# Kernel tuning notes

Hardware: AMD Instinct MI355X
Metric: run time of the kernel (lower is better)

The kernel has to match this reference:

```python
import jax, jax.numpy as jnp
import numpy as np

B, S, D, U = 8, 2048, 512, 512
L0, L1 = 128, 128  # limit_context (left, right)


def setup_inputs() -> dict:
    key = jax.random.key(0)
    ks = jax.random.split(key, 7)
    scale = 1.0 / np.sqrt(D).astype(np.float32)
    return {
        "x": jax.random.normal(ks[0], (B, S, D), dtype=jnp.float32),
        "Wq": jax.random.normal(ks[1], (D, U), dtype=jnp.float32) * scale,
        "Wk": jax.random.normal(ks[2], (D, U), dtype=jnp.float32) * scale,
        "Wv": jax.random.normal(ks[3], (D, U), dtype=jnp.float32) * scale,
        "bq": jnp.zeros((U,), dtype=jnp.float32),
        "bk": jnp.zeros((U,), dtype=jnp.float32),
        "bv": jnp.zeros((U,), dtype=jnp.float32),
    }


def reference(x, Wq, Wk, Wv, bq, bk, bv):
    # Linear projections for query / key / value (shared input x)
    q = x @ Wq + bq  # [B,S,U]
    k = x @ Wk + bk  # [B,S,U]
    v = x @ Wv + bv  # [B,S,U]

    inv_sqrt_dv = jnp.float32(1.0 / np.sqrt(U))
    scores = jnp.einsum("bqd,bkd->bqk", q, k) * inv_sqrt_dv  # [B,S,S]

    # Sliding-window mask: key j visible to query i iff i-L0 <= j <= i+L1.
    # Equivalent to the original per-step softmax over values[:, start:end].
    i = jnp.arange(S)[:, None]
    j = jnp.arange(S)[None, :]
    window = (j >= i - L0) & (j <= i + L1)  # [S,S]
    neg_inf = jnp.finfo(scores.dtype).min
    scores = jnp.where(window[None], scores, neg_inf)

    attn = jax.nn.softmax(scores, axis=-1)  # [B,S,S]
    return jnp.einsum("bqk,bkd->bqd", attn, v)  # [B,S,U]
```

## Files before the change

### kernel.cpp

```cpp
#include <hip/hip_runtime.h>

#define BATCH 8
#define S_LEN 2048
#define DDIM 512
#define UDIM 512
#define WIN_L 128
#define WIN_R 128
#define KP 520
#define VP 40
#define PP 296

typedef _Float16 f16;
typedef __attribute__((ext_vector_type(8))) _Float16 f16x8;
typedef __attribute__((ext_vector_type(4))) _Float16 f16x4;
typedef __attribute__((ext_vector_type(4))) float f32x4;

__device__ __forceinline__ void gload_lds16(const void* g, void* l) {
  __builtin_amdgcn_global_load_lds((const __attribute__((address_space(1))) void*)g,
                                   (__attribute__((address_space(3))) void*)l, 16, 0, 0);
}

__global__ void cast_f32_f16(const float* __restrict__ in, f16* __restrict__ out, int n) {
  int i = (blockIdx.x * blockDim.x + threadIdx.x) * 4;
  if (i < n) {
    float4 v = *(const float4*)(in + i);
    f16x4 o;
    o[0] = (f16)v.x; o[1] = (f16)v.y; o[2] = (f16)v.z; o[3] = (f16)v.w;
    *(f16x4*)(out + i) = o;
  }
}

__global__ void transpose_w(const float* __restrict__ Wq, const float* __restrict__ Wk,
                            const float* __restrict__ Wv, f16* __restrict__ WT) {
  const float* W = blockIdx.z == 0 ? Wq : (blockIdx.z == 1 ? Wk : Wv);
  f16* WTz = WT + (size_t)blockIdx.z * DDIM * UDIM;
  __shared__ float t[32][33];
  int tx = threadIdx.x & 31, ty = threadIdx.x >> 5;
  int n0 = blockIdx.x * 32, k0 = blockIdx.y * 32;
  for (int i = 0; i < 4; i++) {
    int r = ty * 4 + i;
    t[r][tx] = W[(size_t)(k0 + r) * UDIM + n0 + tx];
  }
  __syncthreads();
  for (int i = 0; i < 4; i++) {
    int r = ty * 4 + i;
    WTz[(size_t)(n0 + r) * DDIM + k0 + tx] = (f16)t[tx][r];
  }
}

__global__ __launch_bounds__(256, 2) void gemm_qkv(
    const f16* __restrict__ X, const f16* __restrict__ WT,
    const float* __restrict__ bq, const float* __restrict__ bk, const float* __restrict__ bv,
    f16* __restrict__ QKV, f16* __restrict__ VT) {
  int z = blockIdx.z;
  const f16* WTz = WT + (size_t)z * DDIM * UDIM;
  const float* bias = z == 0 ? bq : (z == 1 ? bk : bv);
  f16* out = QKV + (size_t)z * (BATCH * S_LEN) * UDIM;

  __shared__ f16 Al[2][128 * 32];
  __shared__ f16 Bl[2][128 * 32];

  int tid = threadIdx.x, wv = tid >> 6, ln = tid & 63;
  int m0 = blockIdx.x * 128, n0 = blockIdx.y * 128;
  int wm = (wv >> 1) * 64, wn = (wv & 1) * 64;
  int lm = ln & 15, lq = ln >> 4;
  int srow = ln >> 2, scol = (ln & 3) * 8;

  f32x4 acc[4][4];
  for (int mt = 0; mt < 4; mt++)
    for (int nt = 0; nt < 4; nt++)
      for (int r = 0; r < 4; r++) acc[mt][nt][r] = 0.f;

  for (int k0 = 0; k0 < DDIM; k0 += 64) {
    for (int half = 0; half < 2; half++) {
      int r0 = half * 64 + wv * 16;
      for (int c = 0; c < 2; c++) {
        gload_lds16(X + (size_t)(m0 + r0 + srow) * DDIM + k0 + c * 32 + scol, &Al[c][r0 * 32]);
        gload_lds16(WTz + (size_t)(n0 + r0 + srow) * DDIM + k0 + c * 32 + scol, &Bl[c][r0 * 32]);
      }
    }
    __syncthreads();
#pragma unroll
    for (int c = 0; c < 2; c++) {
      f16x8 af[4], bfr[4];
      for (int mt = 0; mt < 4; mt++) af[mt] = *(const f16x8*)&Al[c][(wm + mt * 16 + lm) * 32 + lq * 8];
      for (int nt = 0; nt < 4; nt++) bfr[nt] = *(const f16x8*)&Bl[c][(wn + nt * 16 + lm) * 32 + lq * 8];
      for (int mt = 0; mt < 4; mt++)
        for (int nt = 0; nt < 4; nt++)
          acc[mt][nt] = __builtin_amdgcn_mfma_f32_16x16x32_f16(af[mt], bfr[nt], acc[mt][nt], 0, 0, 0);
    }
    __syncthreads();
  }

  if (z == 2) {
    for (int mt = 0; mt < 4; mt++)
      for (int nt = 0; nt < 4; nt++) {
        int col = n0 + wn + nt * 16 + lm;
        float bv_ = bias[col];
        int row0 = m0 + wm + mt * 16 + lq * 4;
        int bb = row0 >> 11, ss = row0 & 2047;
        f16x4 o;
        for (int r = 0; r < 4; r++) o[r] = (f16)(acc[mt][nt][r] + bv_);
        *(f16x4*)&VT[((size_t)bb * UDIM + col) * S_LEN + ss] = o;
      }
  } else {
    for (int mt = 0; mt < 4; mt++)
      for (int nt = 0; nt < 4; nt++) {
        int col = n0 + wn + nt * 16 + lm;
        float bv_ = bias[col];
        for (int r = 0; r < 4; r++) {
          int row = m0 + wm + mt * 16 + lq * 4 + r;
          out[(size_t)row * UDIM + col] = (f16)(acc[mt][nt][r] + bv_);
        }
      }
  }
}

__global__ __launch_bounds__(256, 2) void attn(
    const f16* __restrict__ Q, const f16* __restrict__ K, const f16* __restrict__ VT,
    float* __restrict__ out) {
  __shared__ __align__(16) char ubuf[VP * 512 * 2];
  __shared__ f16 Pb[32 * PP];
  __shared__ float wmax[2][32], wsum[2][32];
  f16* Kl = (f16*)ubuf;
  f16* Vl = (f16*)ubuf;

  int tid = threadIdx.x, wv = tid >> 6, ln = tid & 63;
  int lm = ln & 15, lq = ln >> 4;
  int b = blockIdx.x, q0 = blockIdx.y * 32;
  int rh = wv >> 1, kh = wv & 1;
  const size_t base = (size_t)b * S_LEN;
  const int strip0 = q0 - WIN_L;

  f16x8 qf[16];
  {
    const f16* qrow = Q + (base + q0 + rh * 16 + lm) * (size_t)DDIM + lq * 8;
#pragma unroll
    for (int kk = 0; kk < 16; kk++) qf[kk] = *(const f16x8*)(qrow + kk * 32);
  }

  f32x4 sacc[9];
#pragma unroll
  for (int s = 0; s < 9; s++)
    for (int r = 0; r < 4; r++) sacc[s][r] = 0.f;

#pragma unroll
  for (int s = 0; s < 9; s++) {
    int j0 = strip0 + s * 32;
    if (j0 + 31 >= 0 && j0 < S_LEN) {
#pragma unroll
      for (int i = 0; i < 8; i++) {
        int row = wv * 8 + i;
        int key = j0 + row;
        int kc = key < 0 ? 0 : (key > S_LEN - 1 ? S_LEN - 1 : key);
        gload_lds16(K + (base + kc) * (size_t)DDIM + ln * 8, &Kl[row * KP]);
      }
      __syncthreads();
      f32x4 s0, s1;
      for (int r = 0; r < 4; r++) { s0[r] = 0.f; s1[r] = 0.f; }
#pragma unroll
      for (int kk = 0; kk < 16; kk += 2) {
        f16x8 b0 = *(const f16x8*)&Kl[(kh * 16 + lm) * KP + kk * 32 + lq * 8];
        f16x8 b1 = *(const f16x8*)&Kl[(kh * 16 + lm) * KP + (kk + 1) * 32 + lq * 8];
        s0 = __builtin_amdgcn_mfma_f32_16x16x32_f16(qf[kk], b0, s0, 0, 0, 0);
        s1 = __builtin_amdgcn_mfma_f32_16x16x32_f16(qf[kk + 1], b1, s1, 0, 0, 0);
      }
      for (int r = 0; r < 4; r++) sacc[s][r] = s0[r] + s1[r];
      __syncthreads();
    }
  }

  const float scale = 0.044194173824159216f;
  float mx[4] = {-1e30f, -1e30f, -1e30f, -1e30f};
#pragma unroll
  for (int s = 0; s < 9; s++) {
    int kj = strip0 + s * 32 + kh * 16 + lm;
#pragma unroll
    for (int r = 0; r < 4; r++) {
      int qi = q0 + rh * 16 + lq * 4 + r;
      float v = sacc[s][r] * scale;
      bool ok = (kj >= 0) && (kj < S_LEN) && (kj >= qi - WIN_L) && (kj <= qi + WIN_R);
      v = ok ? v : -1e30f;
      sacc[s][r] = v;
      mx[r] = fmaxf(mx[r], v);
    }
  }
#pragma unroll
  for (int r = 0; r < 4; r++) {
    mx[r] = fmaxf(mx[r], __shfl_xor(mx[r], 1));
    mx[r] = fmaxf(mx[r], __shfl_xor(mx[r], 2));
    mx[r] = fmaxf(mx[r], __shfl_xor(mx[r], 4));
    mx[r] = fmaxf(mx[r], __shfl_xor(mx[r], 8));
  }
  if (lm == 0) {
#pragma unroll
    for (int r = 0; r < 4; r++) wmax[kh][rh * 16 + lq * 4 + r] = mx[r];
  }
  __syncthreads();

  float mrow[4], sum[4] = {0.f, 0.f, 0.f, 0.f};
#pragma unroll
  for (int r = 0; r < 4; r++) {
    int row = rh * 16 + lq * 4 + r;
    mrow[r] = fmaxf(wmax[0][row], wmax[1][row]);
  }
#pragma unroll
  for (int s = 0; s < 9; s++) {
#pragma unroll
    for (int r = 0; r < 4; r++) {
      float p = __expf(sacc[s][r] - mrow[r]);
      sum[r] += p;
      Pb[(rh * 16 + lq * 4 + r) * PP + s * 32 + kh * 16 + lm] = (f16)p;
    }
  }
#pragma unroll
  for (int r = 0; r < 4; r++) {
    sum[r] += __shfl_xor(sum[r], 1);
    sum[r] += __shfl_xor(sum[r], 2);
    sum[r] += __shfl_xor(sum[r], 4);
    sum[r] += __shfl_xor(sum[r], 8);
  }
  if (lm == 0) {
#pragma unroll
    for (int r = 0; r < 4; r++) wsum[kh][rh * 16 + lq * 4 + r] = sum[r];
  }
  __syncthreads();

  f32x4 oacc[2][8];
#pragma unroll
  for (int mt = 0; mt < 2; mt++)
    for (int nt = 0; nt < 8; nt++)
      for (int r = 0; r < 4; r++) oacc[mt][nt][r] = 0.f;

  for (int t = 0; t < 9; t++) {
    int j0 = strip0 + t * 32;
    if (j0 + 31 < 0 || j0 >= S_LEN) continue;
#pragma unroll
    for (int i = 0; i < 8; i++) {
      int u = i * 64 + (tid >> 2);
      int c4 = tid & 3;
      int key = j0 + c4 * 8;
      int kc = key < 0 ? 0 : (key > S_LEN - 8 ? S_LEN - 8 : key);
      f16x8 v = *(const f16x8*)(VT + ((size_t)b * UDIM + u) * S_LEN + kc);
      *(f16x8*)&Vl[u * VP + c4 * 8] = v;
    }
    __syncthreads();
    f16x8 pf0 = *(const f16x8*)&Pb[lm * PP + t * 32 + lq * 8];
    f16x8 pf1 = *(const f16x8*)&Pb[(16 + lm) * PP + t * 32 + lq * 8];
#pragma unroll
    for (int nt = 0; nt < 8; nt++) {
      f16x8 vv = *(const f16x8*)&Vl[(wv * 128 + nt * 16 + lm) * VP + lq * 8];
      oacc[0][nt] = __builtin_amdgcn_mfma_f32_16x16x32_f16(pf0, vv, oacc[0][nt], 0, 0, 0);
      oacc[1][nt] = __builtin_amdgcn_mfma_f32_16x16x32_f16(pf1, vv, oacc[1][nt], 0, 0, 0);
    }
    __syncthreads();
  }

  float linv[2][4];
#pragma unroll
  for (int mt = 0; mt < 2; mt++)
    for (int r = 0; r < 4; r++) {
      int row = mt * 16 + lq * 4 + r;
      linv[mt][r] = 1.0f / (wsum[0][row] + wsum[1][row]);
    }
#pragma unroll
  for (int mt = 0; mt < 2; mt++)
    for (int nt = 0; nt < 8; nt++)
      for (int r = 0; r < 4; r++) {
        int row = q0 + mt * 16 + lq * 4 + r;
        int col = wv * 128 + nt * 16 + lm;
        out[(base + row) * (size_t)UDIM + col] = oacc[mt][nt][r] * linv[mt][r];
      }
}

extern "C" void kernel_launch(void* const* d_in, const int* in_sizes, int n_in,
                              void* d_out, int out_size, void* d_ws, size_t ws_size,
                              hipStream_t stream) {
  const float* x  = (const float*)d_in[0];
  const float* Wq = (const float*)d_in[1];
  const float* Wk = (const float*)d_in[2];
  const float* Wv = (const float*)d_in[3];
  const float* bq = (const float*)d_in[4];
  const float* bk = (const float*)d_in[5];
  const float* bv = (const float*)d_in[6];
  float* out = (float*)d_out;

  char* ws = (char*)d_ws;
  const size_t XB_BYTES  = (size_t)BATCH * S_LEN * DDIM * 2;
  const size_t WT_BYTES  = (size_t)3 * DDIM * UDIM * 2;
  const size_t QKV_BYTES = (size_t)3 * BATCH * S_LEN * UDIM * 2;
  f16* xb  = (f16*)ws;
  f16* WT  = (f16*)(ws + XB_BYTES);
  f16* QKV = (f16*)(ws + XB_BYTES + WT_BYTES);
  f16* VT  = (f16*)(ws + XB_BYTES + WT_BYTES + QKV_BYTES);

  int n = BATCH * S_LEN * DDIM;
  cast_f32_f16<<<n / (256 * 4), 256, 0, stream>>>(x, xb, n);
  transpose_w<<<dim3(16, 16, 3), 256, 0, stream>>>(Wq, Wk, Wv, WT);
  gemm_qkv<<<dim3(128, 4, 3), 256, 0, stream>>>(xb, WT, bq, bk, bv, QKV, VT);
  attn<<<dim3(BATCH, S_LEN / 32), 256, 0, stream>>>(
      QKV, QKV + (size_t)BATCH * S_LEN * UDIM, VT, out);
}
```

Measured before the change: 155.0 us.

## Fuse prep kernels, widen GEMM N-tile, prefetch V tiles in attention

Merges the x cast and weight transpose into a single launch to save one kernel launch. Widens the QKV GEMM tile from 128x128 to 128x256, halving grid columns and doubling accumulator registers per wave for more A-tile reuse. In attention, it precomputes valid strip bounds and register-prefetches the next V tile while the current one is consumed, overlapping global loads with MFMA. The larger GEMM accumulator raises register pressure and may hurt occupancy under the 2-block launch bound.

```diff
diff --git a/kernel.cpp b/kernel.cpp
--- a/kernel.cpp
+++ b/kernel.cpp
@@ -20,31 +20,33 @@
                                    (__attribute__((address_space(3))) void*)l, 16, 0, 0);
 }
 
-__global__ void cast_f32_f16(const float* __restrict__ in, f16* __restrict__ out, int n) {
-  int i = (blockIdx.x * blockDim.x + threadIdx.x) * 4;
-  if (i < n) {
-    float4 v = *(const float4*)(in + i);
+__global__ void prep(const float* __restrict__ x, const float* __restrict__ Wq,
+                     const float* __restrict__ Wk, const float* __restrict__ Wv,
+                     f16* __restrict__ xb, f16* __restrict__ WT) {
+  __shared__ float t[32][33];
+  int bid = blockIdx.x;
+  if (bid < 8192) {
+    int i = (bid * 256 + threadIdx.x) * 4;
+    float4 v = *(const float4*)(x + i);
     f16x4 o;
     o[0] = (f16)v.x; o[1] = (f16)v.y; o[2] = (f16)v.z; o[3] = (f16)v.w;
-    *(f16x4*)(out + i) = o;
-  }
-}
-
-__global__ void transpose_w(const float* __restrict__ Wq, const float* __restrict__ Wk,
-                            const float* __restrict__ Wv, f16* __restrict__ WT) {
-  const float* W = blockIdx.z == 0 ? Wq : (blockIdx.z == 1 ? Wk : Wv);
-  f16* WTz = WT + (size_t)blockIdx.z * DDIM * UDIM;
-  __shared__ float t[32][33];
-  int tx = threadIdx.x & 31, ty = threadIdx.x >> 5;
-  int n0 = blockIdx.x * 32, k0 = blockIdx.y * 32;
-  for (int i = 0; i < 4; i++) {
-    int r = ty * 4 + i;
-    t[r][tx] = W[(size_t)(k0 + r) * UDIM + n0 + tx];
-  }
-  __syncthreads();
-  for (int i = 0; i < 4; i++) {
-    int r = ty * 4 + i;
-    WTz[(size_t)(n0 + r) * DDIM + k0 + tx] = (f16)t[tx][r];
+    *(f16x4*)(xb + i) = o;
+  } else {
+    int id = bid - 8192;
+    int zx = id & 15, zy = (id >> 4) & 15, zz = id >> 8;
+    const float* W = zz == 0 ? Wq : (zz == 1 ? Wk : Wv);
+    f16* WTz = WT + (size_t)zz * DDIM * UDIM;
+    int tx = threadIdx.x & 31, ty = threadIdx.x >> 5;
+    int n0 = zx * 32, k0 = zy * 32;
+    for (int i = 0; i < 4; i++) {
+      int r = ty * 4 + i;
+      t[r][tx] = W[(size_t)(k0 + r) * UDIM + n0 + tx];
+    }
+    __syncthreads();
+    for (int i = 0; i < 4; i++) {
+      int r = ty * 4 + i;
+      WTz[(size_t)(n0 + r) * DDIM + k0 + tx] = (f16)t[tx][r];
+    }
   }
 }
 
@@ -58,43 +60,56 @@
   f16* out = QKV + (size_t)z * (BATCH * S_LEN) * UDIM;
 
   __shared__ f16 Al[2][128 * 32];
-  __shared__ f16 Bl[2][128 * 32];
+  __shared__ f16 Bl[2][256 * 32];
 
   int tid = threadIdx.x, wv = tid >> 6, ln = tid & 63;
-  int m0 = blockIdx.x * 128, n0 = blockIdx.y * 128;
-  int wm = (wv >> 1) * 64, wn = (wv & 1) * 64;
+  int m0 = blockIdx.x * 128, n0 = blockIdx.y * 256;
+  int wm = (wv >> 1) * 64, wn = (wv & 1) * 128;
   int lm = ln & 15, lq = ln >> 4;
   int srow = ln >> 2, scol = (ln & 3) * 8;
 
-  f32x4 acc[4][4];
+  f32x4 acc[4][8];
+#pragma unroll
   for (int mt = 0; mt < 4; mt++)
-    for (int nt = 0; nt < 4; nt++)
+    for (int nt = 0; nt < 8; nt++)
       for (int r = 0; r < 4; r++) acc[mt][nt][r] = 0.f;
 
   for (int k0 = 0; k0 < DDIM; k0 += 64) {
-    for (int half = 0; half < 2; half++) {
-      int r0 = half * 64 + wv * 16;
-      for (int c = 0; c < 2; c++) {
+#pragma unroll
+    for (int c = 0; c < 2; c++) {
+#pragma unroll
+      for (int half = 0; half < 2; half++) {
+        int r0 = half * 64 + wv * 16;
         gload_lds16(X + (size_t)(m0 + r0 + srow) * DDIM + k0 + c * 32 + scol, &Al[c][r0 * 32]);
+      }
+#pragma unroll
+      for (int i = 0; i < 4; i++) {
+        int r0 = wv * 64 + i * 16;
         gload_lds16(WTz + (size_t)(n0 + r0 + srow) * DDIM + k0 + c * 32 + scol, &Bl[c][r0 * 32]);
       }
     }
     __syncthreads();
 #pragma unroll
     for (int c = 0; c < 2; c++) {
-      f16x8 af[4], bfr[4];
+      f16x8 af[4], bfr[8];
+#pragma unroll
       for (int mt = 0; mt < 4; mt++) af[mt] = *(const f16x8*)&Al[c][(wm + mt * 16 + lm) * 32 + lq * 8];
-      for (int nt = 0; nt < 4; nt++) bfr[nt] = *(const f16x8*)&Bl[c][(wn + nt * 16 + lm) * 32 + lq * 8];
+#pragma unroll
+      for (int nt = 0; nt < 8; nt++) bfr[nt] = *(const f16x8*)&Bl[c][(wn + nt * 16 + lm) * 32 + lq * 8];
+#pragma unroll
       for (int mt = 0; mt < 4; mt++)
-        for (int nt = 0; nt < 4; nt++)
+#pragma unroll
+        for (int nt = 0; nt < 8; nt++)
           acc[mt][nt] = __builtin_amdgcn_mfma_f32_16x16x32_f16(af[mt], bfr[nt], acc[mt][nt], 0, 0, 0);
     }
     __syncthreads();
   }
 
   if (z == 2) {
+#pragma unroll
     for (int mt = 0; mt < 4; mt++)
-      for (int nt = 0; nt < 4; nt++) {
+#pragma unroll
+      for (int nt = 0; nt < 8; nt++) {
         int col = n0 + wn + nt * 16 + lm;
         float bv_ = bias[col];
         int row0 = m0 + wm + mt * 16 + lq * 4;
@@ -104,8 +119,10 @@
         *(f16x4*)&VT[((size_t)bb * UDIM + col) * S_LEN + ss] = o;
       }
   } else {
+#pragma unroll
     for (int mt = 0; mt < 4; mt++)
-      for (int nt = 0; nt < 4; nt++) {
+#pragma unroll
+      for (int nt = 0; nt < 8; nt++) {
         int col = n0 + wn + nt * 16 + lm;
         float bv_ = bias[col];
         for (int r = 0; r < 4; r++) {
@@ -131,6 +148,8 @@
   int rh = wv >> 1, kh = wv & 1;
   const size_t base = (size_t)b * S_LEN;
   const int strip0 = q0 - WIN_L;
+  const int t_lo = strip0 < 0 ? (-strip0) >> 5 : 0;
+  int t_hi = (S_LEN - strip0) >> 5; if (t_hi > 9) t_hi = 9;
 
   f16x8 qf[16];
   {
@@ -146,8 +165,8 @@
 
 #pragma unroll
   for (int s = 0; s < 9; s++) {
-    int j0 = strip0 + s * 32;
-    if (j0 + 31 >= 0 && j0 < S_LEN) {
+    if (s >= t_lo && s < t_hi) {
+      int j0 = strip0 + s * 32;
 #pragma unroll
       for (int i = 0; i < 8; i++) {
         int row = wv * 8 + i;
@@ -232,26 +251,35 @@
     for (int nt = 0; nt < 8; nt++)
       for (int r = 0; r < 4; r++) oacc[mt][nt][r] = 0.f;
 
-  for (int t = 0; t < 9; t++) {
-    int j0 = strip0 + t * 32;
-    if (j0 + 31 < 0 || j0 >= S_LEN) continue;
-#pragma unroll
-    for (int i = 0; i < 8; i++) {
-      int u = i * 64 + (tid >> 2);
-      int c4 = tid & 3;
-      int key = j0 + c4 * 8;
+  int vu = (tid >> 2), vc4 = tid & 3;
+  const f16* vsrc = VT + ((size_t)b * UDIM + vu) * S_LEN;
+  f16x8 vreg[8];
+  {
+    int j0 = strip0 + t_lo * 32;
+    int key = j0 + vc4 * 8;
+    int kc = key < 0 ? 0 : (key > S_LEN - 8 ? S_LEN - 8 : key);
+#pragma unroll
+    for (int i = 0; i < 8; i++) vreg[i] = *(const f16x8*)(vsrc + (size_t)(i * 64) * S_LEN + kc);
+  }
+
+  for (int t = t_lo; t < t_hi; t++) {
+#pragma unroll
+    for (int i = 0; i < 8; i++) *(f16x8*)&Vl[(i * 64 + vu) * VP + vc4 * 8] = vreg[i];
+    __syncthreads();
+    if (t + 1 < t_hi) {
+      int j0 = strip0 + (t + 1) * 32;
+      int key = j0 + vc4 * 8;
       int kc = key < 0 ? 0 : (key > S_LEN - 8 ? S_LEN - 8 : key);
-      f16x8 v = *(const f16x8*)(VT + ((size_t)b * UDIM + u) * S_LEN + kc);
-      *(f16x8*)&Vl[u * VP + c4 * 8] = v;
-    }
-    __syncthreads();
+#pragma unroll
+      for (int i = 0; i < 8; i++) vreg[i] = *(const f16x8*)(vsrc + (size_t)(i * 64) * S_LEN + kc);
+    }
     f16x8 pf0 = *(const f16x8*)&Pb[lm * PP + t * 32 + lq * 8];
     f16x8 pf1 = *(const f16x8*)&Pb[(16 + lm) * PP + t * 32 + lq * 8];
 #pragma unroll
     for (int nt = 0; nt < 8; nt++) {
-      f16x8 vv = *(const f16x8*)&Vl[(wv * 128 + nt * 16 + lm) * VP + lq * 8];
-      oacc[0][nt] = __builtin_amdgcn_mfma_f32_16x16x32_f16(pf0, vv, oacc[0][nt], 0, 0, 0);
-      oacc[1][nt] = __builtin_amdgcn_mfma_f32_16x16x32_f16(pf1, vv, oacc[1][nt], 0, 0, 0);
+      f16x8 vvf = *(const f16x8*)&Vl[(wv * 128 + nt * 16 + lm) * VP + lq * 8];
+      oacc[0][nt] = __builtin_amdgcn_mfma_f32_16x16x32_f16(pf0, vvf, oacc[0][nt], 0, 0, 0);
+      oacc[1][nt] = __builtin_amdgcn_mfma_f32_16x16x32_f16(pf1, vvf, oacc[1][nt], 0, 0, 0);
     }
     __syncthreads();
   }
@@ -294,10 +322,8 @@
   f16* QKV = (f16*)(ws + XB_BYTES + WT_BYTES);
   f16* VT  = (f16*)(ws + XB_BYTES + WT_BYTES + QKV_BYTES);
 
-  int n = BATCH * S_LEN * DDIM;
-  cast_f32_f16<<<n / (256 * 4), 256, 0, stream>>>(x, xb, n);
-  transpose_w<<<dim3(16, 16, 3), 256, 0, stream>>>(Wq, Wk, Wv, WT);
-  gemm_qkv<<<dim3(128, 4, 3), 256, 0, stream>>>(xb, WT, bq, bk, bv, QKV, VT);
+  prep<<<8192 + 768, 256, 0, stream>>>(x, Wq, Wk, Wv, xb, WT);
+  gemm_qkv<<<dim3(128, 2, 3), 256, 0, stream>>>(xb, WT, bq, bk, bv, QKV, VT);
   attn<<<dim3(BATCH, S_LEN / 32), 256, 0, stream>>>(
       QKV, QKV + (size_t)BATCH * S_LEN * UDIM, VT, out);
 }
```

After: 161.7 us. +4.3%, slower.
